# Performance work log

Hardware: AMD Instinct MI355X
Metric: run time of the kernel (lower is better)

Reference implementation:

```python
import jax, jax.numpy as jnp
import numpy as np
import math

FACTOR = 5

def setup_inputs() -> dict:
    key = jax.random.key(0)
    k1, k2, k3, k4 = jax.random.split(key, 4)
    B, L, H, D = 4, 2048, 8, 64
    sample_k = FACTOR * math.ceil(math.log(L))  # 40
    queries = jax.random.normal(k1, (B, L, H, D), dtype=jnp.float32)
    keys = jax.random.normal(k2, (B, L, H, D), dtype=jnp.float32)
    values = jax.random.normal(k3, (B, L, H, D), dtype=jnp.float32)
    index_sample = jax.random.randint(k4, (L, sample_k), 0, L, dtype=jnp.int32)
    return {"queries": queries, "keys": keys, "values": values, "index_sample": index_sample}

def reference(queries, keys, values, index_sample):
    B, L_Q, H, D = queries.shape
    L_K = keys.shape[1]
    # [B,L,H,D] -> [B,H,L,D]
    Q = jnp.swapaxes(queries, 1, 2)
    K = jnp.swapaxes(keys, 1, 2)
    # values are cumsum'ed along the length axis before attention
    Vc = jnp.cumsum(jnp.swapaxes(values, 1, 2), axis=-2)
    u = min(FACTOR * math.ceil(math.log(L_Q)), L_Q)  # n_top
    # --- _prob_QK ---
    # gather sampled keys per query position: [B,H,L_Q,sample_k,D]
    K_sample = K[:, :, index_sample, :]
    # sampled scores: [B,H,L_Q,sample_k]
    Q_K_sample = jnp.einsum('bhqd,bhqsd->bhqs', Q, K_sample)
    # sparsity measure M = max - mean(scaled by L_K)
    M = Q_K_sample.max(axis=-1) - Q_K_sample.sum(axis=-1) / L_K  # [B,H,L_Q]
    M_top = jax.lax.top_k(M, u)[1]  # [B,H,u] query indices
    # gather top queries: [B,H,u,D]
    Q_reduce = jnp.take_along_axis(Q, M_top[..., None], axis=2)
    # full scores for selected queries: [B,H,u,L_K]
    scores = jnp.einsum('bhud,bhkd->bhuk', Q_reduce, K)
    scale = 1.0 / math.sqrt(D)
    scores = scores * scale
    # mask_flag=False, output_attention=False -> plain softmax then matmul with cumsum'ed V
    attn = jax.nn.softmax(scores, axis=-1)
    context = jnp.einsum('bhuk,bhkd->bhud', attn, Vc)  # [B,H,u,D]
    return context
```

## Files before the change

kernel.cpp:

```cpp
#include <hip/hip_runtime.h>
#include <hip/hip_bf16.h>
#include <math.h>

#define B 4
#define L 2048
#define H 8
#define D 64
#define SK 40
#define U 40
#define JC 32
#define JCL (L / JC)

#define OFF_M    0
#define OFF_TOP  262144
#define OFF_T    270336
#define OFF_PART 10756096

__device__ __forceinline__ float dot4(float4 a, float4 b) {
    return fmaf(a.x, b.x, fmaf(a.y, b.y, fmaf(a.z, b.z, a.w * b.w)));
}

__global__ __launch_bounds__(256) void k_msamp(const float* __restrict__ Q,
                                               const float* __restrict__ K,
                                               const int* __restrict__ idx,
                                               float* __restrict__ M) {
    int g  = blockIdx.x & 7;
    int b  = g >> 1;
    int hh = g & 1;
    int t  = threadIdx.x;
    int wave = t >> 6;
    int lane = t & 63;
    int qp = lane >> 5;
    int hp = (lane >> 3) & 3;
    int c  = lane & 7;
    int h  = hh * 4 + hp;
    int q  = (blockIdx.x >> 3) * 8 + wave * 2 + qp;

    const float* qrow = Q + (size_t)((b * L + q) * H + h) * D + c * 8;
    float4 qa = *(const float4*)qrow;
    float4 qb = *(const float4*)(qrow + 4);

    int s1 = lane & 31;
    int v1 = idx[q * SK + s1];
    int s2 = 32 + s1; if (s2 > SK - 1) s2 = SK - 1;
    int v2 = idx[q * SK + s2];

    const float* kbase = K + (size_t)b * L * H * D + (size_t)h * D + c * 8;

    float vmax = -__builtin_inff();
    float vsum = 0.f;
#pragma unroll 8
    for (int s = 0; s < SK; ++s) {
        int kidx = (s < 32) ? __shfl(v1, qp * 32 + s, 64)
                            : __shfl(v2, qp * 32 + (s - 32), 64);
        const float* kp = kbase + (size_t)kidx * (H * D);
        float4 ka = *(const float4*)kp;
        float4 kb = *(const float4*)(kp + 4);
        float d8 = dot4(qa, ka) + dot4(qb, kb);
        d8 += __shfl_xor(d8, 1, 64);
        d8 += __shfl_xor(d8, 2, 64);
        d8 += __shfl_xor(d8, 4, 64);
        vmax = fmaxf(vmax, d8);
        vsum += d8;
    }
    if (c == 0) M[(size_t)(b * H + h) * L + q] = vmax - vsum * (1.0f / (float)L);
}

__global__ __launch_bounds__(256) void k_topk(const float* __restrict__ M,
                                              int* __restrict__ top) {
    __shared__ unsigned long long cand[L];
    __shared__ unsigned int bins[256];
    __shared__ unsigned int red[256];
    __shared__ int cnt2;

    int bh = blockIdx.x;
    int tid = threadIdx.x;
    const float* m = M + (size_t)bh * L;

    bins[tid] = 0;
    if (tid == 0) cnt2 = 0;

    unsigned int u8[8];
    unsigned int umin = 0xFFFFFFFFu, umax = 0u;
#pragma unroll
    for (int e = 0; e < 8; ++e) {
        int i = tid * 8 + e;
        unsigned int bits = __float_as_uint(m[i]);
        unsigned int u = (bits & 0x80000000u) ? ~bits : (bits | 0x80000000u);
        u8[e] = u;
        umin = min(umin, u);
        umax = max(umax, u);
    }
    red[tid] = umin;
    __syncthreads();
    for (int s = 128; s; s >>= 1) {
        if (tid < s) red[tid] = min(red[tid], red[tid + s]);
        __syncthreads();
    }
    unsigned int kmin = red[0];
    __syncthreads();
    red[tid] = umax;
    __syncthreads();
    for (int s = 128; s; s >>= 1) {
        if (tid < s) red[tid] = max(red[tid], red[tid + s]);
        __syncthreads();
    }
    unsigned int kmax = red[0];
    __syncthreads();

    unsigned int range = kmax - kmin;
    if (range == 0u) {
        if (tid < U) top[bh * U + tid] = tid;
        return;
    }
    int hb = 31 - __clz(range);
    int shift = (hb > 7) ? (hb - 7) : 0;

#pragma unroll
    for (int e = 0; e < 8; ++e) {
        unsigned int bin = (u8[e] - kmin) >> shift;
        atomicAdd(&bins[bin], 1u);
    }
    __syncthreads();

    red[tid] = bins[tid];
    __syncthreads();
    for (int s = 1; s < 256; s <<= 1) {
        unsigned int add = (tid + s < 256) ? red[tid + s] : 0u;
        __syncthreads();
        red[tid] += add;
        __syncthreads();
    }
    int cnt = __syncthreads_count(red[tid] >= U);
    unsigned int t = (unsigned int)(cnt - 1);

#pragma unroll
    for (int e = 0; e < 8; ++e) {
        unsigned int u = u8[e];
        if (((u - kmin) >> shift) >= t) {
            int pos = atomicAdd(&cnt2, 1);
            int i = tid * 8 + e;
            cand[pos] = ((unsigned long long)u << 11) | (unsigned long long)(2047 - i);
        }
    }
    __syncthreads();
    int C = cnt2;

    for (int j = tid; j < C; j += 256) {
        unsigned long long kj = cand[j];
        int r = 0;
        for (int kk = 0; kk < C; ++kk) r += (cand[kk] > kj);
        if (r < U) top[bh * U + r] = 2047 - (int)(kj & 0x7FFull);
    }
}

__global__ __launch_bounds__(256) void k_scores(const float* __restrict__ Q,
                                                const float* __restrict__ K,
                                                const int* __restrict__ top,
                                                float* __restrict__ T) {
    __shared__ float4 sQ4[U * 16];
    int bh = blockIdx.x >> 4;
    int kc = blockIdx.x & 15;
    int b = bh >> 3, h = bh & (H - 1);
    int tid = threadIdx.x;
    int lane = tid & 63;
    int w = tid >> 6;

    for (int i = tid; i < U * 16; i += 256) {
        int u = i >> 4, c = i & 15;
        int qidx = top[bh * U + u];
        sQ4[i] = *((const float4*)(Q + (size_t)((b * L + qidx) * H + h) * D) + c);
    }

    int k0 = kc * 128 + lane;
    const float4* kr0 = (const float4*)(K + (size_t)((b * L + k0) * H + h) * D);
    const float4* kr1 = (const float4*)(K + (size_t)((b * L + k0 + 64) * H + h) * D);
    float4 kv0[16], kv1[16];
#pragma unroll
    for (int i = 0; i < 16; ++i) { kv0[i] = kr0[i]; kv1[i] = kr1[i]; }
    __syncthreads();

    float* Tb = T + (size_t)bh * U * L;
    for (int uu = 0; uu < 10; ++uu) {
        int u = w * 10 + uu;
        float s0 = 0.f, s1 = 0.f;
#pragma unroll
        for (int i = 0; i < 16; ++i) {
            float4 q4 = sQ4[u * 16 + i];
            s0 += dot4(q4, kv0[i]);
            s1 += dot4(q4, kv1[i]);
        }
        Tb[(size_t)u * L + k0]      = s0 * 0.125f;
        Tb[(size_t)u * L + k0 + 64] = s1 * 0.125f;
    }
}

__global__ __launch_bounds__(256) void k_softsuf(float* __restrict__ T) {
    __shared__ float red[256];
    __shared__ float arr[256];
    int row = blockIdx.x;
    float* t = T + (size_t)row * L;
    int tid = threadIdx.x;

    const float4* p = (const float4*)(t + tid * 8);
    float4 a = p[0], c = p[1];
    float x[8] = {a.x, a.y, a.z, a.w, c.x, c.y, c.z, c.w};

    float mx = x[0];
#pragma unroll
    for (int i = 1; i < 8; ++i) mx = fmaxf(mx, x[i]);
    red[tid] = mx;
    __syncthreads();
    for (int s = 128; s; s >>= 1) {
        if (tid < s) red[tid] = fmaxf(red[tid], red[tid + s]);
        __syncthreads();
    }
    float maxv = red[0];
    __syncthreads();

    float e[8];
#pragma unroll
    for (int i = 0; i < 8; ++i) e[i] = __expf(x[i] - maxv);
    float ls[8];
    ls[7] = e[7];
#pragma unroll
    for (int i = 6; i >= 0; --i) ls[i] = e[i] + ls[i + 1];
    float mytotal = ls[0];

    arr[tid] = mytotal;
    __syncthreads();
    for (int s = 1; s < 256; s <<= 1) {
        float add = (tid + s < 256) ? arr[tid + s] : 0.f;
        __syncthreads();
        arr[tid] += add;
        __syncthreads();
    }
    float denom = arr[0];
    float off = arr[tid] - mytotal;
    float r = 1.0f / denom;

    float4 o0 = make_float4((ls[0] + off) * r, (ls[1] + off) * r,
                            (ls[2] + off) * r, (ls[3] + off) * r);
    float4 o1 = make_float4((ls[4] + off) * r, (ls[5] + off) * r,
                            (ls[6] + off) * r, (ls[7] + off) * r);
    float4* po = (float4*)(t + tid * 8);
    po[0] = o0; po[1] = o1;
}

__global__ __launch_bounds__(256) void k_ctx(const float* __restrict__ V,
                                             const float* __restrict__ T,
                                             float* __restrict__ part) {
    __shared__ float sT[U][JCL];
    int bh = blockIdx.x >> 5;
    int jc = blockIdx.x & 31;
    int b = bh >> 3, h = bh & (H - 1);
    int tid = threadIdx.x;
    int w = tid >> 6;
    int lane = tid & 63;
    int j2 = lane >> 4;
    int d4 = lane & 15;

    const float* Tg = T + (size_t)bh * U * L + jc * JCL;
    float4* sT4 = (float4*)sT;
    for (int i = tid; i < U * (JCL / 4); i += 256) {
        int u = i >> 4, cc = i & 15;
        sT4[i] = ((const float4*)(Tg + (size_t)u * L))[cc];
    }
    __syncthreads();

    float4 acc[10];
#pragma unroll
    for (int uu = 0; uu < 10; ++uu) acc[uu] = make_float4(0.f, 0.f, 0.f, 0.f);

    const float* Vb = V + (size_t)(b * L) * (H * D) + (size_t)h * D + d4 * 4;
#pragma unroll 4
    for (int it = 0; it < JCL / 4; ++it) {
        int j = it * 4 + j2;
        float4 v4 = *(const float4*)(Vb + (size_t)(jc * JCL + j) * (H * D));
#pragma unroll
        for (int uu = 0; uu < 10; ++uu) {
            float tj = sT[w * 10 + uu][j];
            acc[uu].x = fmaf(tj, v4.x, acc[uu].x);
            acc[uu].y = fmaf(tj, v4.y, acc[uu].y);
            acc[uu].z = fmaf(tj, v4.z, acc[uu].z);
            acc[uu].w = fmaf(tj, v4.w, acc[uu].w);
        }
    }

    float* po = part + ((size_t)jc * (B * H) + bh) * (U * D);
#pragma unroll
    for (int uu = 0; uu < 10; ++uu) {
        float4 a = acc[uu];
        a.x += __shfl_xor(a.x, 16, 64); a.y += __shfl_xor(a.y, 16, 64);
        a.z += __shfl_xor(a.z, 16, 64); a.w += __shfl_xor(a.w, 16, 64);
        a.x += __shfl_xor(a.x, 32, 64); a.y += __shfl_xor(a.y, 32, 64);
        a.z += __shfl_xor(a.z, 32, 64); a.w += __shfl_xor(a.w, 32, 64);
        if (j2 == 0) *(float4*)(po + (w * 10 + uu) * D + d4 * 4) = a;
    }
}

__global__ __launch_bounds__(256) void k_red(const float* __restrict__ part,
                                             float* __restrict__ out) {
    int o = blockIdx.x * 256 + threadIdx.x;
    if (o >= B * H * U * D) return;
    int bh = o / (U * D);
    int rest = o - bh * (U * D);
    float s = 0.f;
#pragma unroll
    for (int jc = 0; jc < JC; ++jc)
        s += part[(size_t)(jc * (B * H) + bh) * (U * D) + rest];
    out[o] = s;
}

extern "C" void kernel_launch(void* const* d_in, const int* in_sizes, int n_in,
                              void* d_out, int out_size, void* d_ws, size_t ws_size,
                              hipStream_t stream) {
    const float* Q  = (const float*)d_in[0];
    const float* K  = (const float*)d_in[1];
    const float* V  = (const float*)d_in[2];
    const int* idx  = (const int*)d_in[3];
    float* out = (float*)d_out;

    float* M    = (float*)((char*)d_ws + OFF_M);
    int*   top  = (int*)  ((char*)d_ws + OFF_TOP);
    float* T    = (float*)((char*)d_ws + OFF_T);
    float* part = (float*)((char*)d_ws + OFF_PART);

    k_msamp<<<(L / 8) * 8, 256, 0, stream>>>(Q, K, idx, M);
    k_topk<<<B * H, 256, 0, stream>>>(M, top);
    k_scores<<<B * H * 16, 256, 0, stream>>>(Q, K, top, T);
    k_softsuf<<<B * H * U, 256, 0, stream>>>(T);
    k_ctx<<<B * H * JC, 256, 0, stream>>>(V, T, part);
    k_red<<<(B * H * U * D + 255) / 256, 256, 0, stream>>>(part, out);
}
```

Measured before the change: 156.5 us.

## Fuse exp into score kernel and compute suffix sums via chunk tails

Result: faster. 150.0 us (-4.2%).

```diff
diff --git a/kernel.cpp b/kernel.cpp
--- a/kernel.cpp
+++ b/kernel.cpp
@@ -11,10 +11,13 @@
 #define JC 32
 #define JCL (L / JC)
 
-#define OFF_M    0
-#define OFF_TOP  262144
-#define OFF_T    270336
-#define OFF_PART 10756096
+#define OFF_M     0
+#define OFF_TOP   262144
+#define OFF_T     270336
+#define OFF_PART  10756096
+#define OFF_CSUM  21241856
+#define OFF_TAILS 21405696
+#define OFF_RDEN  21569536
 
 __device__ __forceinline__ float dot4(float4 a, float4 b) {
     return fmaf(a.x, b.x, fmaf(a.y, b.y, fmaf(a.z, b.z, a.w * b.w)));
@@ -80,12 +83,14 @@
     bins[tid] = 0;
     if (tid == 0) cnt2 = 0;
 
+    const float4* m4 = (const float4*)(m + tid * 8);
+    float4 fa = m4[0], fb = m4[1];
+    float f8[8] = {fa.x, fa.y, fa.z, fa.w, fb.x, fb.y, fb.z, fb.w};
     unsigned int u8[8];
     unsigned int umin = 0xFFFFFFFFu, umax = 0u;
 #pragma unroll
     for (int e = 0; e < 8; ++e) {
-        int i = tid * 8 + e;
-        unsigned int bits = __float_as_uint(m[i]);
+        unsigned int bits = __float_as_uint(f8[e]);
         unsigned int u = (bits & 0x80000000u) ? ~bits : (bits | 0x80000000u);
         u8[e] = u;
         umin = min(umin, u);
@@ -157,7 +162,8 @@
 __global__ __launch_bounds__(256) void k_scores(const float* __restrict__ Q,
                                                 const float* __restrict__ K,
                                                 const int* __restrict__ top,
-                                                float* __restrict__ T) {
+                                                float* __restrict__ T,
+                                                float* __restrict__ csum) {
     __shared__ float4 sQ4[U * 16];
     int bh = blockIdx.x >> 4;
     int kc = blockIdx.x & 15;
@@ -190,65 +196,43 @@
             s0 += dot4(q4, kv0[i]);
             s1 += dot4(q4, kv1[i]);
         }
-        Tb[(size_t)u * L + k0]      = s0 * 0.125f;
-        Tb[(size_t)u * L + k0 + 64] = s1 * 0.125f;
-    }
-}
-
-__global__ __launch_bounds__(256) void k_softsuf(float* __restrict__ T) {
-    __shared__ float red[256];
-    __shared__ float arr[256];
-    int row = blockIdx.x;
-    float* t = T + (size_t)row * L;
-    int tid = threadIdx.x;
-
-    const float4* p = (const float4*)(t + tid * 8);
-    float4 a = p[0], c = p[1];
-    float x[8] = {a.x, a.y, a.z, a.w, c.x, c.y, c.z, c.w};
-
-    float mx = x[0];
-#pragma unroll
-    for (int i = 1; i < 8; ++i) mx = fmaxf(mx, x[i]);
-    red[tid] = mx;
-    __syncthreads();
-    for (int s = 128; s; s >>= 1) {
-        if (tid < s) red[tid] = fmaxf(red[tid], red[tid + s]);
-        __syncthreads();
-    }
-    float maxv = red[0];
-    __syncthreads();
-
-    float e[8];
-#pragma unroll
-    for (int i = 0; i < 8; ++i) e[i] = __expf(x[i] - maxv);
-    float ls[8];
-    ls[7] = e[7];
-#pragma unroll
-    for (int i = 6; i >= 0; --i) ls[i] = e[i] + ls[i + 1];
-    float mytotal = ls[0];
-
-    arr[tid] = mytotal;
-    __syncthreads();
-    for (int s = 1; s < 256; s <<= 1) {
-        float add = (tid + s < 256) ? arr[tid + s] : 0.f;
-        __syncthreads();
-        arr[tid] += add;
-        __syncthreads();
-    }
-    float denom = arr[0];
-    float off = arr[tid] - mytotal;
-    float r = 1.0f / denom;
-
-    float4 o0 = make_float4((ls[0] + off) * r, (ls[1] + off) * r,
-                            (ls[2] + off) * r, (ls[3] + off) * r);
-    float4 o1 = make_float4((ls[4] + off) * r, (ls[5] + off) * r,
-                            (ls[6] + off) * r, (ls[7] + off) * r);
-    float4* po = (float4*)(t + tid * 8);
-    po[0] = o0; po[1] = o1;
+        float e0 = __expf(s0 * 0.125f);
+        float e1 = __expf(s1 * 0.125f);
+        Tb[(size_t)u * L + k0]      = e0;
+        Tb[(size_t)u * L + k0 + 64] = e1;
+        float c0 = e0, c1 = e1;
+#pragma unroll
+        for (int o = 1; o < 64; o <<= 1) {
+            c0 += __shfl_xor(c0, o, 64);
+            c1 += __shfl_xor(c1, o, 64);
+        }
+        if (lane == 0) {
+            csum[((size_t)bh * U + u) * JC + 2 * kc]     = c0;
+            csum[((size_t)bh * U + u) * JC + 2 * kc + 1] = c1;
+        }
+    }
+}
+
+__global__ __launch_bounds__(64) void k_tails(const float* __restrict__ csum,
+                                              float* __restrict__ tails,
+                                              float* __restrict__ rden) {
+    int bh = blockIdx.x;
+    int r = threadIdx.x;
+    if (r < U) {
+        size_t base = ((size_t)bh * U + r) * JC;
+        float acc = 0.f;
+#pragma unroll
+        for (int j = JC - 1; j >= 0; --j) {
+            tails[base + j] = acc;
+            acc += csum[base + j];
+        }
+        rden[bh * U + r] = 1.0f / acc;
+    }
 }
 
 __global__ __launch_bounds__(256) void k_ctx(const float* __restrict__ V,
-                                             const float* __restrict__ T,
+                                             const float* __restrict__ E,
+                                             const float* __restrict__ tails,
                                              float* __restrict__ part) {
     __shared__ float sT[U][JCL];
     int bh = blockIdx.x >> 5;
@@ -260,11 +244,18 @@
     int j2 = lane >> 4;
     int d4 = lane & 15;
 
-    const float* Tg = T + (size_t)bh * U * L + jc * JCL;
-    float4* sT4 = (float4*)sT;
-    for (int i = tid; i < U * (JCL / 4); i += 256) {
-        int u = i >> 4, cc = i & 15;
-        sT4[i] = ((const float4*)(Tg + (size_t)u * L))[cc];
+    const float* Eg = E + (size_t)bh * U * L + jc * JCL;
+#pragma unroll
+    for (int r = 0; r < 10; ++r) {
+        int u = w * 10 + r;
+        float v = Eg[(size_t)u * L + lane];
+#pragma unroll
+        for (int s = 1; s < 64; s <<= 1) {
+            float o = __shfl_down(v, s, 64);
+            v += (lane + s < 64) ? o : 0.f;
+        }
+        v += tails[((size_t)bh * U + u) * JC + jc];
+        sT[u][lane] = v;
     }
     __syncthreads();
 
@@ -300,16 +291,18 @@
 }
 
 __global__ __launch_bounds__(256) void k_red(const float* __restrict__ part,
+                                             const float* __restrict__ rden,
                                              float* __restrict__ out) {
     int o = blockIdx.x * 256 + threadIdx.x;
     if (o >= B * H * U * D) return;
     int bh = o / (U * D);
     int rest = o - bh * (U * D);
+    int u = rest >> 6;
     float s = 0.f;
 #pragma unroll
     for (int jc = 0; jc < JC; ++jc)
         s += part[(size_t)(jc * (B * H) + bh) * (U * D) + rest];
-    out[o] = s;
+    out[o] = s * rden[bh * U + u];
 }
 
 extern "C" void kernel_launch(void* const* d_in, const int* in_sizes, int n_in,
@@ -321,15 +314,18 @@
     const int* idx  = (const int*)d_in[3];
     float* out = (float*)d_out;
 
-    float* M    = (float*)((char*)d_ws + OFF_M);
-    int*   top  = (int*)  ((char*)d_ws + OFF_TOP);
-    float* T    = (float*)((char*)d_ws + OFF_T);
-    float* part = (float*)((char*)d_ws + OFF_PART);
+    float* M     = (float*)((char*)d_ws + OFF_M);
+    int*   top   = (int*)  ((char*)d_ws + OFF_TOP);
+    float* T     = (float*)((char*)d_ws + OFF_T);
+    float* part  = (float*)((char*)d_ws + OFF_PART);
+    float* csum  = (float*)((char*)d_ws + OFF_CSUM);
+    float* tails = (float*)((char*)d_ws + OFF_TAILS);
+    float* rden  = (float*)((char*)d_ws + OFF_RDEN);
 
     k_msamp<<<(L / 8) * 8, 256, 0, stream>>>(Q, K, idx, M);
     k_topk<<<B * H, 256, 0, stream>>>(M, top);
-    k_scores<<<B * H * 16, 256, 0, stream>>>(Q, K, top, T);
-    k_softsuf<<<B * H * U, 256, 0, stream>>>(T);
-    k_ctx<<<B * H * JC, 256, 0, stream>>>(V, T, part);
-    k_red<<<(B * H * U * D + 255) / 256, 256, 0, stream>>>(part, out);
-}
+    k_scores<<<B * H * 16, 256, 0, stream>>>(Q, K, top, T, csum);
+    k_tails<<<B * H, 64, 0, stream>>>(csum, tails, rden);
+    k_ctx<<<B * H * JC, 256, 0, stream>>>(V, T, tails, part);
+    k_red<<<(B * H * U * D + 255) / 256, 256, 0, stream>>>(part, rden, out);
+}
```
